# Optimization experiments

Measured on AMD Instinct MI355X. Metric: run time of the kernel, lower is better.

## Reference

```python
import jax, jax.numpy as jnp
import numpy as np

C = 256
C8 = C // 8

def setup_inputs() -> dict:
    key = jax.random.key(0)
    ks = jax.random.split(key, 8)
    a = jax.random.normal(ks[0], (4, C, 64, 64), dtype=jnp.float32)
    s = 1.0 / np.sqrt(C)
    b_w = jax.random.normal(ks[1], (C8, C), dtype=jnp.float32) * s
    b_b = jnp.zeros((C8,), dtype=jnp.float32)
    c_w = jax.random.normal(ks[2], (C8, C), dtype=jnp.float32) * s
    c_b = jnp.zeros((C8,), dtype=jnp.float32)
    d_w = jax.random.normal(ks[3], (C, C), dtype=jnp.float32) * s
    d_b = jnp.zeros((C,), dtype=jnp.float32)
    alpha = jnp.zeros((1,), dtype=jnp.float32) + 0.5  # nonzero so attention path is exercised
    return {"a": a, "b_w": b_w, "b_b": b_b, "c_w": c_w, "c_b": c_b, "d_w": d_w, "d_b": d_b, "alpha": alpha}

def _conv1x1(x, w, b):
    # x: [n, c, h, w], w: [o, c] -> [n, o, h, w]
    return jnp.einsum('nchw,oc->nohw', x, w) + b[None, :, None, None]

def reference(a, b_w, b_b, c_w, c_b, d_w, d_b, alpha):
    n, chan, h, w = a.shape
    nhw = h * w
    b = _conv1x1(a, b_w, b_b).reshape(n, -1, nhw)   # [n, C/8, nhw]
    c = _conv1x1(a, c_w, c_b).reshape(n, -1, nhw)   # [n, C/8, nhw]
    k = jnp.einsum('nci,ncj->nij', b, c)            # [n, nhw, nhw]
    s = jax.nn.softmax(k, axis=-1)
    d = _conv1x1(a, d_w, d_b).reshape(n, -1, nhw)   # [n, C, nhw]
    kl = jnp.einsum('ncj,nij->nci', d, s)           # d @ s^T
    kl = kl.reshape(n, chan, h, w)
    return alpha * kl + a
```

## Files before the change

### kernel.cpp

```cpp
#include <hip/hip_runtime.h>
#include <hip/hip_bf16.h>

#define CCH 256
#define CQK 32
#define NHW 4096

typedef float f32x4 __attribute__((ext_vector_type(4)));
typedef _Float16 hv8 __attribute__((ext_vector_type(8)));
typedef _Float16 hv4 __attribute__((ext_vector_type(4)));
typedef __fp16 fv2 __attribute__((ext_vector_type(2)));

typedef __attribute__((address_space(3))) unsigned int lds_u32_t;
typedef __attribute__((address_space(1))) const unsigned int glb_u32_t;
__device__ __forceinline__ void gll16(const _Float16* gp, _Float16* lp) {
    __builtin_amdgcn_global_load_lds((glb_u32_t*)gp, (lds_u32_t*)lp, 16, 0, 0);
}

__global__ __launch_bounds__(256) void prep_kernel(
    const float* __restrict__ b_w, const float* __restrict__ c_w,
    const float* __restrict__ d_w, _Float16* __restrict__ Wh)
{
    const int bid = blockIdx.x, tid = threadIdx.x;
    const int idx = (bid * 256 + tid) * 4;
    const int row = idx >> 8, col = idx & 255;
    const float* src = (row < 32) ? (b_w + row * CCH + col)
                     : (row < 64) ? (c_w + (row - 32) * CCH + col)
                                  : (d_w + (row - 64) * CCH + col);
    const float scl = (row < 32) ? 1.4426950408889634f : 1.0f;
    float4 v = *reinterpret_cast<const float4*>(src);
    _Float16* dst = Wh + (size_t)row * CCH + col;
    dst[0] = (_Float16)(v.x * scl); dst[1] = (_Float16)(v.y * scl);
    dst[2] = (_Float16)(v.z * scl); dst[3] = (_Float16)(v.w * scl);
}

__global__ __launch_bounds__(256) void proj_kernel(
    const float* __restrict__ a, const _Float16* __restrict__ Wh,
    const float* __restrict__ b_b, const float* __restrict__ c_b,
    const float* __restrict__ d_b,
    _Float16* __restrict__ bqT, _Float16* __restrict__ ckT,
    _Float16* __restrict__ dv)
{
    __shared__ _Float16 aT[32][CCH + 24];

    const int n    = blockIdx.x >> 7;
    const int i0   = (blockIdx.x & 127) << 5;
    const int tid  = threadIdx.x;
    const int lane = tid & 63;
    const int wave = tid >> 6;
    const int l15  = lane & 15;
    const int quad = lane >> 4;

    {
        const float* ap = a + (size_t)(n*CCH + tid)*NHW + i0;
        #pragma unroll
        for (int j = 0; j < 8; ++j) {
            float4 v = *reinterpret_cast<const float4*>(ap + j*4);
            aT[j*4+0][tid] = (_Float16)v.x;
            aT[j*4+1][tid] = (_Float16)v.y;
            aT[j*4+2][tid] = (_Float16)v.z;
            aT[j*4+3][tid] = (_Float16)v.w;
        }
    }
    __syncthreads();

    const f32x4 zf = {0.f, 0.f, 0.f, 0.f};
    f32x4 acc[5][2];
    #pragma unroll
    for (int t = 0; t < 5; ++t) { acc[t][0] = zf; acc[t][1] = zf; }

    const int ch0w = wave * 80;

    #pragma unroll
    for (int ks = 0; ks < 8; ++ks) {
        const int k0 = ks * 32;
        hv8 af0 = *reinterpret_cast<const hv8*>(&aT[l15][k0 + quad*8]);
        hv8 af1 = *reinterpret_cast<const hv8*>(&aT[16 + l15][k0 + quad*8]);
        #pragma unroll
        for (int t = 0; t < 5; ++t) {
            const int ch0 = ch0w + t*16;
            hv8 bf = *reinterpret_cast<const hv8*>(
                Wh + (size_t)(ch0 + l15)*CCH + k0 + quad*8);
            acc[t][0] = __builtin_amdgcn_mfma_f32_16x16x32_f16(af0, bf, acc[t][0], 0, 0, 0);
            acc[t][1] = __builtin_amdgcn_mfma_f32_16x16x32_f16(af1, bf, acc[t][1], 0, 0, 0);
        }
    }

    const int pos_b = i0 + quad*4;
    #pragma unroll
    for (int t = 0; t < 5; ++t) {
        const int ch0 = ch0w + t*16;
        if (ch0 < 64) {
            const float* bias_arr = (ch0 < 32) ? b_b : c_b;
            _Float16*    outp     = (ch0 < 32) ? bqT : ckT;
            const int    ch       = (ch0 & 31) + l15;
            const float  bias     = bias_arr[ch] *
                ((ch0 < 32) ? 1.4426950408889634f : 1.0f);
            #pragma unroll
            for (int nf = 0; nf < 2; ++nf) {
                #pragma unroll
                for (int r = 0; r < 4; ++r) {
                    const int pos = pos_b + nf*16 + r;
                    outp[((size_t)n*NHW + pos)*CQK + ch] =
                        (_Float16)(acc[t][nf][r] + bias);
                }
            }
        } else {
            const int ch   = ch0 - 64 + l15;
            const float bias = d_b[ch];
            #pragma unroll
            for (int nf = 0; nf < 2; ++nf) {
                hv4 v = { (_Float16)(acc[t][nf][0] + bias),
                          (_Float16)(acc[t][nf][1] + bias),
                          (_Float16)(acc[t][nf][2] + bias),
                          (_Float16)(acc[t][nf][3] + bias) };
                *reinterpret_cast<hv4*>(
                    dv + ((size_t)n*CCH + ch)*NHW + pos_b + nf*16) = v;
            }
        }
    }
}

__global__ __launch_bounds__(512, 2) void attn_kernel(
    const _Float16* __restrict__ bqT, const _Float16* __restrict__ ckT,
    const _Float16* __restrict__ dv,
    const float* __restrict__ a, const float* __restrict__ alpha_p,
    float* __restrict__ out)
{
    __shared__ __align__(16) char smem[141312];

    const int bx   = ((blockIdx.x & 7) << 5) | (blockIdx.x >> 3);
    const int n    = bx >> 6;
    const int cg   = (bx >> 5) & 1;
    const int qt   = bx & 31;
    const int q0b  = qt << 7;
    const int co0  = cg << 7;
    const int tid  = threadIdx.x;
    const int wave = tid >> 6;
    const int g    = wave >> 1;
    const int qw   = wave & 1;
    const int lane = tid & 63;
    const int l15  = lane & 15;
    const int quad = lane >> 4;
    const int kg0  = g << 10;

    _Float16* vbuf = (_Float16*)(smem + (g << 14));
    _Float16* pb   = (_Float16*)(smem + 65536 + wave*9216);
    float*    lbuf = (float*)(smem + 139264);

    const f32x4 zf = {0.f, 0.f, 0.f, 0.f};
    const _Float16 one_h = (_Float16)1.0f;
    const hv8 ones = { one_h, one_h, one_h, one_h, one_h, one_h, one_h, one_h };

    hv8 qf[4];
    #pragma unroll
    for (int X = 0; X < 4; ++X) {
        const int q = q0b + qw*64 + X*16 + l15;
        qf[X] = *reinterpret_cast<const hv8*>(
            bqT + ((size_t)n*NHW + q)*CQK + quad*8);
    }

    const _Float16* ckbase = ckT + ((size_t)(n*NHW + kg0 + l15))*CQK + quad*8;

    float mneg[4];
    {
        float mx[4];
        #pragma unroll
        for (int X = 0; X < 4; ++X) mx[X] = -1e30f;
        for (int kt = 0; kt < 16; ++kt) {
            #pragma unroll
            for (int f = 0; f < 4; ++f) {
                hv8 kf = *reinterpret_cast<const hv8*>(
                    ckbase + (size_t)(kt*64 + f*16)*CQK);
                #pragma unroll
                for (int X = 0; X < 4; ++X) {
                    f32x4 s = __builtin_amdgcn_mfma_f32_16x16x32_f16(
                        kf, qf[X], zf, 0, 0, 0);
                    mx[X] = fmaxf(mx[X],
                        fmaxf(fmaxf(s[0], s[1]), fmaxf(s[2], s[3])));
                }
            }
        }
        #pragma unroll
        for (int X = 0; X < 4; ++X) {
            mx[X] = fmaxf(mx[X], __shfl_xor(mx[X], 16, 64));
            mx[X] = fmaxf(mx[X], __shfl_xor(mx[X], 32, 64));
        }
        if (lane < 16) {
            #pragma unroll
            for (int X = 0; X < 4; ++X)
                lbuf[(g*2 + qw)*64 + X*16 + l15] = mx[X];
        }
        __syncthreads();
        #pragma unroll
        for (int X = 0; X < 4; ++X) {
            const int qi = qw*64 + X*16 + l15;
            float m0 = lbuf[(0*2 + qw)*64 + X*16 + l15];
            float m1 = lbuf[(1*2 + qw)*64 + X*16 + l15];
            float m2 = lbuf[(2*2 + qw)*64 + X*16 + l15];
            float m3 = lbuf[(3*2 + qw)*64 + X*16 + l15];
            (void)qi;
            mneg[X] = -fmaxf(fmaxf(m0, m1), fmaxf(m2, m3));
        }
        __syncthreads();
    }

    f32x4 acc[4][8];
    #pragma unroll
    for (int X = 0; X < 4; ++X)
        #pragma unroll
        for (int t = 0; t < 8; ++t) acc[X][t] = zf;
    f32x4 accL[4];
    #pragma unroll
    for (int X = 0; X < 4; ++X) accL[X] = zf;

    const int rl8 = lane >> 3;
    const _Float16* dvs = dv
        + (size_t)(n*CCH + co0 + qw*64 + rl8)*NHW + kg0 + 8*((lane & 7) ^ rl8);
    _Float16* ldsb = (_Float16*)(smem + (g << 14) + qw*8192);

    const int c0h = ((quad*16) ^ ((l15 & 7) << 4)) >> 1;
    const int c1h = ((64 + quad*16) ^ ((l15 & 7) << 4)) >> 1;

    auto softmax_tile = [&](const hv8* kf) {
        #pragma unroll
        for (int X = 0; X < 4; ++X) {
            const f32x4 minit = {mneg[X], mneg[X], mneg[X], mneg[X]};
            #pragma unroll
            for (int f = 0; f < 4; ++f) {
                f32x4 s = __builtin_amdgcn_mfma_f32_16x16x32_f16(
                    kf[f], qf[X], minit, 0, 0, 0);
                float p0 = __builtin_amdgcn_exp2f(s[0]);
                float p1 = __builtin_amdgcn_exp2f(s[1]);
                float p2 = __builtin_amdgcn_exp2f(s[2]);
                float p3 = __builtin_amdgcn_exp2f(s[3]);
                fv2 lo = __builtin_amdgcn_cvt_pkrtz(p0, p1);
                fv2 hi = __builtin_amdgcn_cvt_pkrtz(p2, p3);
                uint2 w;
                w.x = __builtin_bit_cast(unsigned, lo);
                w.y = __builtin_bit_cast(unsigned, hi);
                *reinterpret_cast<uint2*>(
                    pb + X*1152 + l15*72 + f*16 + quad*4) = w;
            }
        }
    };

    hv8 pf0[4], pf1[4];
    auto read_pf = [&]() {
        #pragma unroll
        for (int X = 0; X < 4; ++X) {
            pf0[X] = *reinterpret_cast<const hv8*>(pb + X*1152 + l15*72 + quad*8);
            pf1[X] = *reinterpret_cast<const hv8*>(pb + X*1152 + l15*72 + 32 + quad*8);
        }
    };

    auto stage = [&](int kt) {
        #pragma unroll
        for (int j = 0; j < 8; ++j)
            gll16(dvs + (size_t)(j*8)*NHW + kt*64, ldsb + (size_t)(j*8)*64);
    };

    auto load_kf = [&](int key0, hv8* kf) {
        #pragma unroll
        for (int f = 0; f < 4; ++f)
            kf[f] = *reinterpret_cast<const hv8*>(
                ckbase + (size_t)(key0 + f*16)*CQK);
    };

    {
        stage(0);
        hv8 kf0[4];
        load_kf(0, kf0);
        softmax_tile(kf0);
        read_pf();
    }
    __syncthreads();

    for (int kt = 0; kt < 16; ++kt) {
        hv8 kfn[4];
        if (kt < 15) load_kf((kt + 1)*64, kfn);

        #pragma unroll
        for (int t = 0; t < 8; ++t) {
            const _Float16* vr = vbuf + (t*16 + l15)*64;
            hv8 d0 = *reinterpret_cast<const hv8*>(vr + c0h);
            #pragma unroll
            for (int X = 0; X < 4; ++X)
                acc[X][t] = __builtin_amdgcn_mfma_f32_16x16x32_f16(
                    pf0[X], d0, acc[X][t], 0, 0, 0);
            hv8 d1 = *reinterpret_cast<const hv8*>(vr + c1h);
            #pragma unroll
            for (int X = 0; X < 4; ++X)
                acc[X][t] = __builtin_amdgcn_mfma_f32_16x16x32_f16(
                    pf1[X], d1, acc[X][t], 0, 0, 0);
        }
        #pragma unroll
        for (int X = 0; X < 4; ++X) {
            accL[X] = __builtin_amdgcn_mfma_f32_16x16x32_f16(pf0[X], ones, accL[X], 0, 0, 0);
            accL[X] = __builtin_amdgcn_mfma_f32_16x16x32_f16(pf1[X], ones, accL[X], 0, 0, 0);
        }

        if (kt < 15) {
            softmax_tile(kfn);
            __syncthreads();
            stage(kt + 1);
            read_pf();
            __syncthreads();
        }
    }

    __syncthreads();
    float* buf1 = (float*)smem;
    float* buf2 = (float*)(smem + 67584);

    if (l15 == 0) {
        #pragma unroll
        for (int X = 0; X < 4; ++X)
            *reinterpret_cast<float4*>(&lbuf[g*128 + qw*64 + X*16 + quad*4]) =
                *reinterpret_cast<float4*>(&accL[X]);
    }
    if (g == 1 || g == 3) {
        float* b = (g == 1) ? buf1 : buf2;
        #pragma unroll
        for (int X = 0; X < 4; ++X)
            #pragma unroll
            for (int t = 0; t < 8; ++t)
                *reinterpret_cast<float4*>(
                    &b[(t*16 + l15)*132 + qw*64 + X*16 + quad*4]) =
                    *reinterpret_cast<float4*>(&acc[X][t]);
    }
    __syncthreads();
    if (g == 0 || g == 2) {
        float* b = (g == 0) ? buf1 : buf2;
        #pragma unroll
        for (int X = 0; X < 4; ++X)
            #pragma unroll
            for (int t = 0; t < 8; ++t) {
                float4 p = *reinterpret_cast<float4*>(
                    &b[(t*16 + l15)*132 + qw*64 + X*16 + quad*4]);
                acc[X][t][0] += p.x; acc[X][t][1] += p.y;
                acc[X][t][2] += p.z; acc[X][t][3] += p.w;
            }
    }
    __syncthreads();
    if (g == 2) {
        #pragma unroll
        for (int X = 0; X < 4; ++X)
            #pragma unroll
            for (int t = 0; t < 8; ++t)
                *reinterpret_cast<float4*>(
                    &buf1[(t*16 + l15)*132 + qw*64 + X*16 + quad*4]) =
                    *reinterpret_cast<float4*>(&acc[X][t]);
    }
    __syncthreads();
    if (g == 0) {
        const float alpha = alpha_p[0];
        #pragma unroll
        for (int X = 0; X < 4; ++X) {
            const int qloc = qw*64 + X*16 + quad*4;
            #pragma unroll
            for (int t = 0; t < 8; ++t) {
                float4 p = *reinterpret_cast<float4*>(
                    &buf1[(t*16 + l15)*132 + qloc]);
                acc[X][t][0] += p.x; acc[X][t][1] += p.y;
                acc[X][t][2] += p.z; acc[X][t][3] += p.w;
            }
            float4 l0 = *reinterpret_cast<float4*>(&lbuf[0*128 + qloc]);
            float4 l1 = *reinterpret_cast<float4*>(&lbuf[1*128 + qloc]);
            float4 l2 = *reinterpret_cast<float4*>(&lbuf[2*128 + qloc]);
            float4 l3 = *reinterpret_cast<float4*>(&lbuf[3*128 + qloc]);
            f32x4 rl;
            rl[0] = alpha / (l0.x + l1.x + l2.x + l3.x);
            rl[1] = alpha / (l0.y + l1.y + l2.y + l3.y);
            rl[2] = alpha / (l0.z + l1.z + l2.z + l3.z);
            rl[3] = alpha / (l0.w + l1.w + l2.w + l3.w);
            #pragma unroll
            for (int t = 0; t < 8; ++t) {
                const size_t off =
                    ((size_t)(n*CCH + co0 + t*16 + l15))*NHW + q0b + qloc;
                float4 av = *reinterpret_cast<const float4*>(a + off);
                float4 o;
                o.x = acc[X][t][0]*rl[0] + av.x;
                o.y = acc[X][t][1]*rl[1] + av.y;
                o.z = acc[X][t][2]*rl[2] + av.z;
                o.w = acc[X][t][3]*rl[3] + av.w;
                *reinterpret_cast<float4*>(out + off) = o;
            }
        }
    }
}

extern "C" void kernel_launch(void* const* d_in, const int* in_sizes, int n_in,
                              void* d_out, int out_size, void* d_ws, size_t ws_size,
                              hipStream_t stream)
{
    const float* a    = (const float*)d_in[0];
    const float* b_w  = (const float*)d_in[1];
    const float* b_b  = (const float*)d_in[2];
    const float* c_w  = (const float*)d_in[3];
    const float* c_b  = (const float*)d_in[4];
    const float* d_w  = (const float*)d_in[5];
    const float* d_b  = (const float*)d_in[6];
    const float* alp  = (const float*)d_in[7];
    float* out = (float*)d_out;

    _Float16* bqT  = (_Float16*)d_ws;
    _Float16* ckT  = bqT + (size_t)4*NHW*CQK;
    _Float16* dv   = ckT + (size_t)4*NHW*CQK;
    _Float16* Wh   = dv + (size_t)4*CCH*NHW;

    prep_kernel<<<80, 256, 0, stream>>>(b_w, c_w, d_w, Wh);
    proj_kernel<<<512, 256, 0, stream>>>(a, Wh, b_b, c_b, d_b, bqT, ckT, dv);
    attn_kernel<<<256, 512, 0, stream>>>(bqT, ckT, dv, a, alp, out);
}
```

Measured before the change: 165.5 us.

## Replace max pre-pass with lazy online-softmax rescaling and cross-group max merge

```diff
diff --git a/kernel.cpp b/kernel.cpp
--- a/kernel.cpp
+++ b/kernel.cpp
@@ -126,7 +126,7 @@
     const float* __restrict__ a, const float* __restrict__ alpha_p,
     float* __restrict__ out)
 {
-    __shared__ __align__(16) char smem[141312];
+    __shared__ __align__(16) char smem[143360];
 
     const int bx   = ((blockIdx.x & 7) << 5) | (blockIdx.x >> 3);
     const int n    = bx >> 6;
@@ -146,6 +146,7 @@
     _Float16* vbuf = (_Float16*)(smem + (g << 14));
     _Float16* pb   = (_Float16*)(smem + 65536 + wave*9216);
     float*    lbuf = (float*)(smem + 139264);
+    float*    mbuf = (float*)(smem + 141312);
 
     const f32x4 zf = {0.f, 0.f, 0.f, 0.f};
     const _Float16 one_h = (_Float16)1.0f;
@@ -161,48 +162,7 @@
 
     const _Float16* ckbase = ckT + ((size_t)(n*NHW + kg0 + l15))*CQK + quad*8;
 
-    float mneg[4];
-    {
-        float mx[4];
-        #pragma unroll
-        for (int X = 0; X < 4; ++X) mx[X] = -1e30f;
-        for (int kt = 0; kt < 16; ++kt) {
-            #pragma unroll
-            for (int f = 0; f < 4; ++f) {
-                hv8 kf = *reinterpret_cast<const hv8*>(
-                    ckbase + (size_t)(kt*64 + f*16)*CQK);
-                #pragma unroll
-                for (int X = 0; X < 4; ++X) {
-                    f32x4 s = __builtin_amdgcn_mfma_f32_16x16x32_f16(
-                        kf, qf[X], zf, 0, 0, 0);
-                    mx[X] = fmaxf(mx[X],
-                        fmaxf(fmaxf(s[0], s[1]), fmaxf(s[2], s[3])));
-                }
-            }
-        }
-        #pragma unroll
-        for (int X = 0; X < 4; ++X) {
-            mx[X] = fmaxf(mx[X], __shfl_xor(mx[X], 16, 64));
-            mx[X] = fmaxf(mx[X], __shfl_xor(mx[X], 32, 64));
-        }
-        if (lane < 16) {
-            #pragma unroll
-            for (int X = 0; X < 4; ++X)
-                lbuf[(g*2 + qw)*64 + X*16 + l15] = mx[X];
-        }
-        __syncthreads();
-        #pragma unroll
-        for (int X = 0; X < 4; ++X) {
-            const int qi = qw*64 + X*16 + l15;
-            float m0 = lbuf[(0*2 + qw)*64 + X*16 + l15];
-            float m1 = lbuf[(1*2 + qw)*64 + X*16 + l15];
-            float m2 = lbuf[(2*2 + qw)*64 + X*16 + l15];
-            float m3 = lbuf[(3*2 + qw)*64 + X*16 + l15];
-            (void)qi;
-            mneg[X] = -fmaxf(fmaxf(m0, m1), fmaxf(m2, m3));
-        }
-        __syncthreads();
-    }
+    float mneg[4] = {0.f, 0.f, 0.f, 0.f};
 
     f32x4 acc[4][8];
     #pragma unroll
@@ -225,14 +185,44 @@
         #pragma unroll
         for (int X = 0; X < 4; ++X) {
             const f32x4 minit = {mneg[X], mneg[X], mneg[X], mneg[X]};
+            f32x4 s0 = __builtin_amdgcn_mfma_f32_16x16x32_f16(kf[0], qf[X], minit, 0, 0, 0);
+            f32x4 s1 = __builtin_amdgcn_mfma_f32_16x16x32_f16(kf[1], qf[X], minit, 0, 0, 0);
+            f32x4 s2 = __builtin_amdgcn_mfma_f32_16x16x32_f16(kf[2], qf[X], minit, 0, 0, 0);
+            f32x4 s3 = __builtin_amdgcn_mfma_f32_16x16x32_f16(kf[3], qf[X], minit, 0, 0, 0);
+            float tm = fmaxf(
+                fmaxf(fmaxf(fmaxf(s0[0], s0[1]), fmaxf(s0[2], s0[3])),
+                      fmaxf(fmaxf(s1[0], s1[1]), fmaxf(s1[2], s1[3]))),
+                fmaxf(fmaxf(fmaxf(s2[0], s2[1]), fmaxf(s2[2], s2[3])),
+                      fmaxf(fmaxf(s3[0], s3[1]), fmaxf(s3[2], s3[3]))));
+            tm = fmaxf(tm, __shfl_xor(tm, 16, 64));
+            tm = fmaxf(tm, __shfl_xor(tm, 32, 64));
+            const float upd = (tm > 8.0f) ? tm : 0.0f;
+            if (__any(upd > 0.0f)) {
+                const float sc = __builtin_amdgcn_exp2f(-upd);
+                float s_r0 = __shfl(sc, quad*4 + 0, 64);
+                float s_r1 = __shfl(sc, quad*4 + 1, 64);
+                float s_r2 = __shfl(sc, quad*4 + 2, 64);
+                float s_r3 = __shfl(sc, quad*4 + 3, 64);
+                #pragma unroll
+                for (int t = 0; t < 8; ++t) {
+                    acc[X][t][0] *= s_r0; acc[X][t][1] *= s_r1;
+                    acc[X][t][2] *= s_r2; acc[X][t][3] *= s_r3;
+                }
+                accL[X][0] *= s_r0; accL[X][1] *= s_r1;
+                accL[X][2] *= s_r2; accL[X][3] *= s_r3;
+                mneg[X] -= upd;
+                s0[0] -= upd; s0[1] -= upd; s0[2] -= upd; s0[3] -= upd;
+                s1[0] -= upd; s1[1] -= upd; s1[2] -= upd; s1[3] -= upd;
+                s2[0] -= upd; s2[1] -= upd; s2[2] -= upd; s2[3] -= upd;
+                s3[0] -= upd; s3[1] -= upd; s3[2] -= upd; s3[3] -= upd;
+            }
+            const f32x4 sv[4] = {s0, s1, s2, s3};
             #pragma unroll
             for (int f = 0; f < 4; ++f) {
-                f32x4 s = __builtin_amdgcn_mfma_f32_16x16x32_f16(
-                    kf[f], qf[X], minit, 0, 0, 0);
-                float p0 = __builtin_amdgcn_exp2f(s[0]);
-                float p1 = __builtin_amdgcn_exp2f(s[1]);
-                float p2 = __builtin_amdgcn_exp2f(s[2]);
-                float p3 = __builtin_amdgcn_exp2f(s[3]);
+                float p0 = __builtin_amdgcn_exp2f(sv[f][0]);
+                float p1 = __builtin_amdgcn_exp2f(sv[f][1]);
+                float p2 = __builtin_amdgcn_exp2f(sv[f][2]);
+                float p3 = __builtin_amdgcn_exp2f(sv[f][3]);
                 fv2 lo = __builtin_amdgcn_cvt_pkrtz(p0, p1);
                 fv2 hi = __builtin_amdgcn_cvt_pkrtz(p2, p3);
                 uint2 w;
@@ -308,9 +298,44 @@
         }
     }
 
-    __syncthreads();
+    if (lane < 16) {
+        #pragma unroll
+        for (int X = 0; X < 4; ++X)
+            mbuf[g*128 + qw*64 + X*16 + l15] = -mneg[X];
+    }
+    __syncthreads();
+
+    {
+        #pragma unroll
+        for (int X = 0; X < 4; ++X) {
+            const int qloc = qw*64 + X*16 + quad*4;
+            float4 m0 = *reinterpret_cast<float4*>(&mbuf[0*128 + qloc]);
+            float4 m1 = *reinterpret_cast<float4*>(&mbuf[1*128 + qloc]);
+            float4 m2 = *reinterpret_cast<float4*>(&mbuf[2*128 + qloc]);
+            float4 m3 = *reinterpret_cast<float4*>(&mbuf[3*128 + qloc]);
+            float4 mm;
+            mm.x = fmaxf(fmaxf(m0.x, m1.x), fmaxf(m2.x, m3.x));
+            mm.y = fmaxf(fmaxf(m0.y, m1.y), fmaxf(m2.y, m3.y));
+            mm.z = fmaxf(fmaxf(m0.z, m1.z), fmaxf(m2.z, m3.z));
+            mm.w = fmaxf(fmaxf(m0.w, m1.w), fmaxf(m2.w, m3.w));
+            float4 mo = (g == 0) ? m0 : (g == 1) ? m1 : (g == 2) ? m2 : m3;
+            float sc0 = __builtin_amdgcn_exp2f(mo.x - mm.x);
+            float sc1 = __builtin_amdgcn_exp2f(mo.y - mm.y);
+            float sc2 = __builtin_amdgcn_exp2f(mo.z - mm.z);
+            float sc3 = __builtin_amdgcn_exp2f(mo.w - mm.w);
+            #pragma unroll
+            for (int t = 0; t < 8; ++t) {
+                acc[X][t][0] *= sc0; acc[X][t][1] *= sc1;
+                acc[X][t][2] *= sc2; acc[X][t][3] *= sc3;
+            }
+            accL[X][0] *= sc0; accL[X][1] *= sc1;
+            accL[X][2] *= sc2; accL[X][3] *= sc3;
+        }
+    }
+
     float* buf1 = (float*)smem;
     float* buf2 = (float*)(smem + 67584);
+    const int qloc = qw*64 + quad*4;
 
     if (l15 == 0) {
         #pragma unroll
@@ -356,18 +381,18 @@
         const float alpha = alpha_p[0];
         #pragma unroll
         for (int X = 0; X < 4; ++X) {
-            const int qloc = qw*64 + X*16 + quad*4;
+            const int qlocX = qw*64 + X*16 + quad*4;
             #pragma unroll
             for (int t = 0; t < 8; ++t) {
                 float4 p = *reinterpret_cast<float4*>(
-                    &buf1[(t*16 + l15)*132 + qloc]);
+                    &buf1[(t*16 + l15)*132 + qlocX]);
                 acc[X][t][0] += p.x; acc[X][t][1] += p.y;
                 acc[X][t][2] += p.z; acc[X][t][3] += p.w;
             }
-            float4 l0 = *reinterpret_cast<float4*>(&lbuf[0*128 + qloc]);
-            float4 l1 = *reinterpret_cast<float4*>(&lbuf[1*128 + qloc]);
-            float4 l2 = *reinterpret_cast<float4*>(&lbuf[2*128 + qloc]);
-            float4 l3 = *reinterpret_cast<float4*>(&lbuf[3*128 + qloc]);
+            float4 l0 = *reinterpret_cast<float4*>(&lbuf[0*128 + qlocX]);
+            float4 l1 = *reinterpret_cast<float4*>(&lbuf[1*128 + qlocX]);
+            float4 l2 = *reinterpret_cast<float4*>(&lbuf[2*128 + qlocX]);
+            float4 l3 = *reinterpret_cast<float4*>(&lbuf[3*128 + qlocX]);
             f32x4 rl;
             rl[0] = alpha / (l0.x + l1.x + l2.x + l3.x);
             rl[1] = alpha / (l0.y + l1.y + l2.y + l3.y);
@@ -376,7 +401,7 @@
             #pragma unroll
             for (int t = 0; t < 8; ++t) {
                 const size_t off =
-                    ((size_t)(n*CCH + co0 + t*16 + l15))*NHW + q0b + qloc;
+                    ((size_t)(n*CCH + co0 + t*16 + l15))*NHW + q0b + qlocX;
                 float4 av = *reinterpret_cast<const float4*>(a + off);
                 float4 o;
                 o.x = acc[X][t][0]*rl[0] + av.x;
```

Result: no change. 165.0 us (-0.3%).
